# Performance work log

Measured on AMD Instinct MI355X. Metric: run time of the kernel, lower is better.

## Reference

```python
import jax, jax.numpy as jnp
import numpy as np

B, T, D_IN, D_H, N_H = 8, 1024, 512, 64, 8
PAD_TAIL = 128


def setup_inputs() -> dict:
    key = jax.random.key(0)
    ks = jax.random.split(key, 7)
    keys = jax.random.normal(ks[0], (B, T, D_IN), jnp.float32)
    queries = jax.random.normal(ks[1], (B, T, D_IN), jnp.float32)
    values = jax.random.normal(ks[2], (B, T, D_IN), jnp.float32)
    # truncated_normal(stddev=0.01) in the original; plain normal*0.01 is a faithful stand-in
    Wk = jax.random.normal(ks[3], (D_IN, D_H, N_H), jnp.float32) * 0.01
    Wq = jax.random.normal(ks[4], (D_IN, D_H, N_H), jnp.float32) * 0.01
    Wv = jax.random.normal(ks[5], (D_IN, D_H, N_H), jnp.float32) * 0.01
    key_seq = jax.random.randint(ks[6], (B, T), 0, 32000)
    key_seq = key_seq.at[:, -PAD_TAIL:].set(-1)  # -1 marks padding positions
    return {"keys": keys, "queries": queries, "values": values,
            "Wk": Wk, "Wq": Wq, "Wv": Wv, "key_seq": key_seq}


def reference(keys, queries, values, Wk, Wq, Wv, key_seq):
    # projections: (b, t, i) x (i, d, h) -> (b, t, d, h)
    Kh = jnp.einsum('bti,idh->btdh', keys, Wk)
    Qh = jnp.einsum('bti,idh->btdh', queries, Wq)
    Vh = jnp.einsum('bti,idh->btdh', values, Wv)

    # scores: i indexes keys, j indexes queries -> (b, Tk, Tq, h)
    scores = jnp.einsum('bidh,bjdh->bijh', Kh, Qh)

    dt = scores.dtype
    # padding mask over key positions (key_seq == -1 -> -1000)
    pad_mask = (-1000.0 * (1.0 - jnp.sign(key_seq + 1).astype(dt)))[:, :, None, None]
    # causal mask: disallow key index i > query index j (matrix_band_part(_, 0, -1) keeps i<=j)
    Tk, Tq = Kh.shape[1], Qh.shape[1]
    caus_mask = -1000.0 * jnp.tril(jnp.ones((Tk, Tq), dt), k=-1)
    mask = pad_mask + caus_mask[None, :, :, None]

    # NB: original adds mask BEFORE scaling, so the -1000 is also scaled. Keep that order.
    hidden_size = Kh.shape[2]
    scores = (scores + mask) / (hidden_size ** 0.5)

    # softmax over the key axis (axis=1)
    attn = jax.nn.softmax(scores, axis=1)

    # aggregate values: (b, i, j, h) x (b, i, d, h) -> (b, j, d, h)
    h_t = jnp.einsum('bijh,bidh->bjdh', attn, Vh)

    # tf.concat(tf.split(h_t, H, axis=-1), axis=2)[:, :, :, 0]
    # == per-head feature blocks laid out head-major along the feature axis
    b, j, d, nh = h_t.shape
    return h_t.transpose(0, 1, 3, 2).reshape(b, j, nh * d)
```

## Files before the change

### kernel.cpp

```cpp
#include <hip/hip_runtime.h>
#include <hip/hip_bf16.h>

#define B_SZ 8
#define T_SZ 1024
#define D_IN 512
#define D_H  64
#define N_H  8

typedef __hip_bfloat16 bf16;
using short8  = __attribute__((ext_vector_type(8))) short;
using short4v = __attribute__((ext_vector_type(4))) short;
using f32x4   = __attribute__((ext_vector_type(4))) float;

__device__ __forceinline__ unsigned short f2bf(float f) {
    union { __hip_bfloat16 b; unsigned short u; } c;
    c.b = __float2bfloat16(f);
    return c.u;
}

__global__ __launch_bounds__(256) void wt_kernel(
    const float* __restrict__ Wk, const float* __restrict__ Wq,
    const float* __restrict__ Wv, unsigned short* __restrict__ Wt)
{
    const int mat = blockIdx.y;
    const float* W = (mat == 0) ? Wk : (mat == 1) ? Wq : Wv;
    int idx = blockIdx.x * 256 + threadIdx.x;
    float v = W[idx];
    int k = idx >> 9, c = idx & 511;
    int h = c & 7, d = c >> 3;
    Wt[(((size_t)mat * 8 + h) * 64 + d) * 512 + k] = f2bf(v);
}

__global__ __launch_bounds__(256, 3) void proj_kernel(
    const float* __restrict__ keys, const float* __restrict__ queries,
    const float* __restrict__ values,
    const unsigned short* __restrict__ Wt, unsigned short* __restrict__ KQVb)
{
    const int tid = threadIdx.x;
    const int m0  = blockIdx.x * 128;
    const int n0  = blockIdx.y * 128;
    const int mat = blockIdx.z;

    const float* X = (mat == 0) ? keys : (mat == 1) ? queries : values;
    const unsigned short* WT = Wt + (size_t)mat * (512 * 512);
    unsigned short* P = KQVb + (size_t)mat * ((size_t)B_SZ * N_H * T_SZ * D_H);

    __shared__ __align__(16) unsigned short Xst[128 * 72];
    __shared__ __align__(16) unsigned short Wst[128 * 72];

    const int wid = tid >> 6, lane = tid & 63;
    const int quad = lane >> 4, l15 = lane & 15;
    const int wr = (wid >> 1) * 64, wc = (wid & 1) * 64;

    f32x4 acc[4][4];
    #pragma unroll
    for (int i = 0; i < 4; ++i)
        #pragma unroll
        for (int n = 0; n < 4; ++n) acc[i][n] = (f32x4){0.f, 0.f, 0.f, 0.f};

    const float4* X4 = (const float4*)X;

    for (int kc = 0; kc < 8; ++kc) {
        const int k0 = kc * 64;
        __syncthreads();
        #pragma unroll
        for (int q2 = 0; q2 < 8; ++q2) {
            int e = tid + q2 * 256;
            int r = e >> 4, c4 = e & 15;
            float4 v = X4[(size_t)(m0 + r) * (D_IN / 4) + (k0 >> 2) + c4];
            short4v s = {(short)f2bf(v.x), (short)f2bf(v.y),
                         (short)f2bf(v.z), (short)f2bf(v.w)};
            *(short4v*)&Xst[r * 72 + c4 * 4] = s;
        }
        #pragma unroll
        for (int q2 = 0; q2 < 4; ++q2) {
            int e = tid + q2 * 256;
            int row = e >> 3, ch = e & 7;
            *(short8*)&Wst[row * 72 + ch * 8] =
                *(const short8*)&WT[(size_t)(n0 + row) * 512 + k0 + ch * 8];
        }
        __syncthreads();
        #pragma unroll
        for (int ic = 0; ic < 2; ++ic) {
            short8 af[4], bf[4];
            #pragma unroll
            for (int mt = 0; mt < 4; ++mt)
                af[mt] = *(const short8*)&Xst[(wr + mt*16 + l15) * 72 + ic*32 + quad*8];
            #pragma unroll
            for (int nt = 0; nt < 4; ++nt)
                bf[nt] = *(const short8*)&Wst[(wc + nt*16 + l15) * 72 + ic*32 + quad*8];
            #pragma unroll
            for (int mt = 0; mt < 4; ++mt)
                #pragma unroll
                for (int nt = 0; nt < 4; ++nt)
                    acc[mt][nt] = __builtin_amdgcn_mfma_f32_16x16x32_bf16(
                        af[mt], bf[nt], acc[mt][nt], 0, 0, 0);
        }
    }

    #pragma unroll
    for (int mt = 0; mt < 4; ++mt)
        #pragma unroll
        for (int r = 0; r < 4; ++r) {
            int mrow = m0 + wr + mt * 16 + quad * 4 + r;
            int bb = mrow >> 10, t = mrow & 1023;
            #pragma unroll
            for (int nt = 0; nt < 4; ++nt) {
                int c = n0 + wc + nt * 16 + l15;
                int h = c >> 6, d = c & 63;
                P[(((size_t)(bb * N_H + h)) * T_SZ + t) * D_H + d] =
                    f2bf(acc[mt][nt][r]);
            }
        }
}

#define SCALE  0.18033688f
#define MASKV -180.33688f

__global__ __launch_bounds__(512, 4) void attn_kernel(
    const unsigned short* __restrict__ Qb, const unsigned short* __restrict__ Kb,
    const unsigned short* __restrict__ Vb,
    const int* __restrict__ key_seq, float* __restrict__ out)
{
    const int tid  = threadIdx.x;
    const int bid  = blockIdx.x;
    const int pair = bid >> 6;
    const int b    = (bid >> 3) & 7;
    const int h    = bid & 7;
    const int wid  = tid >> 6, lane = tid & 63;
    const int quad = lane >> 4, l15 = lane & 15;

    __shared__ __align__(16) unsigned short Kst[2][64 * 72];
    __shared__ __align__(16) unsigned short VTst[2][64 * 72];
    __shared__ __align__(16) float spadf[2][64];
    __shared__ int tflags[16];

    const size_t bh = (size_t)(b * N_H + h) * T_SZ;

    const int strip_j0 = (wid < 4) ? (15 - pair) * 64 : pair * 64;
    const int j0w = strip_j0 + (wid & 3) * 16;
    const int jg  = j0w + l15;
    const int ntmax = 16 - pair;

    short8 qf0 = *(const short8*)&Qb[(bh + jg) * D_H + quad * 8];
    short8 qf1 = *(const short8*)&Qb[(bh + jg) * D_H + 32 + quad * 8];

    {
        int ka  = key_seq[b * T_SZ + wid * 64 + lane];
        int kb2 = key_seq[b * T_SZ + 512 + wid * 64 + lane];
        unsigned long long ba  = __ballot(ka  != -1);
        unsigned long long bb2 = __ballot(kb2 != -1);
        if (lane == 0) {
            tflags[wid]     = (ba  != 0ull ? 1 : 0) | (ba  != ~0ull ? 2 : 0);
            tflags[8 + wid] = (bb2 != 0ull ? 1 : 0) | (bb2 != ~0ull ? 2 : 0);
        }
    }

    const int sk_row = tid >> 3, sk_c = tid & 7;
    const int sv_i = lane, sv_ch = wid;
    const int sv_col = (sv_i & 3) | ((sv_i & 16) >> 2) | ((sv_i & 4) << 1)
                     | ((sv_i & 8) << 1) | (sv_i & 32);

    short8 kreg = *(const short8*)&Kb[(bh + sk_row) * D_H + sk_c * 8];
    short8 vreg = *(const short8*)&Vb[(bh + sv_i) * D_H + sv_ch * 8];
    int ksv = (tid < 64) ? key_seq[b * T_SZ + tid] : -1;

    __syncthreads();

    unsigned tmask = 1u, pmask = 0u;
    #pragma unroll
    for (int t = 0; t < 16; ++t) {
        int f = tflags[t];
        tmask |= (unsigned)(f & 1) << t;
        pmask |= (unsigned)((f >> 1) & 1) << t;
    }
    tmask &= (unsigned)((1ull << ntmax) - 1ull);
    tmask |= 1u;

    *(short8*)&Kst[0][sk_row * 72 + sk_c * 8] = kreg;
    #pragma unroll
    for (int e = 0; e < 8; ++e)
        VTst[0][(sv_ch * 8 + e) * 72 + sv_col] = (unsigned short)vreg[e];
    if (tid < 64) spadf[0][tid] = (ksv == -1) ? MASKV : 0.f;
    __syncthreads();

    float m = -1e30f, l = 0.f;
    f32x4 o0 = {0.f,0.f,0.f,0.f}, o1 = o0, o2 = o0, o3 = o0;

    unsigned rem = tmask & ~1u;
    int tcur = 0, nb = 0;
    for (;;) {
        int tnext = -1;
        if (rem) { tnext = __ffs((int)rem) - 1; rem &= rem - 1; }
        if (tnext >= 0) {
            const size_t r0 = bh + tnext * 64;
            kreg = *(const short8*)&Kb[(r0 + sk_row) * D_H + sk_c * 8];
            vreg = *(const short8*)&Vb[(r0 + sv_i) * D_H + sv_ch * 8];
            if (tid < 64) ksv = key_seq[b * T_SZ + tnext * 64 + tid];
        }

        const int i0 = tcur * 64;
        if (i0 <= j0w + 15) {
            const bool haspad = (pmask >> tcur) & 1u;
            const bool needC  = (i0 + 63 > j0w);
            float sv[16];
            #pragma unroll
            for (int it = 0; it < 4; ++it) {
                f32x4 s = {0.f,0.f,0.f,0.f};
                short8 a0 = *(const short8*)&Kst[nb][(it*16 + l15) * 72 + quad*8];
                s = __builtin_amdgcn_mfma_f32_16x16x32_bf16(a0, qf0, s, 0, 0, 0);
                short8 a1 = *(const short8*)&Kst[nb][(it*16 + l15) * 72 + 32 + quad*8];
                s = __builtin_amdgcn_mfma_f32_16x16x32_bf16(a1, qf1, s, 0, 0, 0);
                f32x4 sp = {0.f,0.f,0.f,0.f};
                if (haspad) sp = *(const f32x4*)&spadf[nb][it*16 + quad*4];
                #pragma unroll
                for (int r = 0; r < 4; ++r) {
                    float v = __builtin_fmaf(s[r], SCALE, sp[r]);
                    if (needC && (i0 + it*16 + quad*4 + r > jg)) v += MASKV;
                    sv[it*4 + r] = v;
                }
            }

            float mt = sv[0];
            #pragma unroll
            for (int k = 1; k < 16; ++k) mt = fmaxf(mt, sv[k]);
            mt = fmaxf(mt, __shfl_xor(mt, 16));
            mt = fmaxf(mt, __shfl_xor(mt, 32));
            const float mnew  = fmaxf(m, mt);
            const float alpha = exp2f(m - mnew);
            float p[16], ls = 0.f;
            #pragma unroll
            for (int k = 0; k < 16; ++k) {
                p[k] = exp2f(sv[k] - mnew);
                ls += p[k];
            }
            ls += __shfl_xor(ls, 16);
            ls += __shfl_xor(ls, 32);
            l = l * alpha + ls;
            m = mnew;
            o0 *= alpha; o1 *= alpha; o2 *= alpha; o3 *= alpha;

            short8 pf0, pf1;
            #pragma unroll
            for (int e = 0; e < 8; ++e) {
                pf0[e] = (short)f2bf(p[e]);
                pf1[e] = (short)f2bf(p[8 + e]);
            }
            short8 a;
            a = *(const short8*)&VTst[nb][(     l15) * 72 +      quad * 8];
            o0 = __builtin_amdgcn_mfma_f32_16x16x32_bf16(a, pf0, o0, 0, 0, 0);
            a = *(const short8*)&VTst[nb][(     l15) * 72 + 32 + quad * 8];
            o0 = __builtin_amdgcn_mfma_f32_16x16x32_bf16(a, pf1, o0, 0, 0, 0);
            a = *(const short8*)&VTst[nb][(16 + l15) * 72 +      quad * 8];
            o1 = __builtin_amdgcn_mfma_f32_16x16x32_bf16(a, pf0, o1, 0, 0, 0);
            a = *(const short8*)&VTst[nb][(16 + l15) * 72 + 32 + quad * 8];
            o1 = __builtin_amdgcn_mfma_f32_16x16x32_bf16(a, pf1, o1, 0, 0, 0);
            a = *(const short8*)&VTst[nb][(32 + l15) * 72 +      quad * 8];
            o2 = __builtin_amdgcn_mfma_f32_16x16x32_bf16(a, pf0, o2, 0, 0, 0);
            a = *(const short8*)&VTst[nb][(32 + l15) * 72 + 32 + quad * 8];
            o2 = __builtin_amdgcn_mfma_f32_16x16x32_bf16(a, pf1, o2, 0, 0, 0);
            a = *(const short8*)&VTst[nb][(48 + l15) * 72 +      quad * 8];
            o3 = __builtin_amdgcn_mfma_f32_16x16x32_bf16(a, pf0, o3, 0, 0, 0);
            a = *(const short8*)&VTst[nb][(48 + l15) * 72 + 32 + quad * 8];
            o3 = __builtin_amdgcn_mfma_f32_16x16x32_bf16(a, pf1, o3, 0, 0, 0);
        }

        if (tnext < 0) break;

        const int nb2 = nb ^ 1;
        *(short8*)&Kst[nb2][sk_row * 72 + sk_c * 8] = kreg;
        #pragma unroll
        for (int e = 0; e < 8; ++e)
            VTst[nb2][(sv_ch * 8 + e) * 72 + sv_col] = (unsigned short)vreg[e];
        if (tid < 64) spadf[nb2][tid] = (ksv == -1) ? MASKV : 0.f;
        __syncthreads();
        tcur = tnext; nb = nb2;
    }

    const float inv = 1.f / l;
    float* op = out + ((size_t)b * T_SZ + jg) * (N_H * D_H) + h * D_H + quad * 4;
    *(f32x4*)(op +  0) = o0 * inv;
    *(f32x4*)(op + 16) = o1 * inv;
    *(f32x4*)(op + 32) = o2 * inv;
    *(f32x4*)(op + 48) = o3 * inv;
}

extern "C" void kernel_launch(void* const* d_in, const int* in_sizes, int n_in,
                              void* d_out, int out_size, void* d_ws, size_t ws_size,
                              hipStream_t stream) {
    const float* keys    = (const float*)d_in[0];
    const float* queries = (const float*)d_in[1];
    const float* values  = (const float*)d_in[2];
    const float* Wk      = (const float*)d_in[3];
    const float* Wq      = (const float*)d_in[4];
    const float* Wv      = (const float*)d_in[5];
    const int*   key_seq = (const int*)d_in[6];

    const size_t per = (size_t)B_SZ * N_H * T_SZ * D_H;
    unsigned short* KQVb = (unsigned short*)d_ws;
    unsigned short* Kb = KQVb;
    unsigned short* Qb = KQVb + per;
    unsigned short* Vb = KQVb + 2 * per;
    unsigned short* Wt = KQVb + 3 * per;

    wt_kernel<<<dim3(512 * 512 / 256, 3), 256, 0, stream>>>(Wk, Wq, Wv, Wt);
    proj_kernel<<<dim3(64, 4, 3), 256, 0, stream>>>(
        keys, queries, values, Wt, KQVb);
    attn_kernel<<<dim3(512), dim3(512), 0, stream>>>(
        Qb, Kb, Vb, key_seq, (float*)d_out);
}
```

Measured before the change: 156.5 us.

## Double-buffer projection GEMM with direct-to-LDS weight loads and swizzled LDS

Restructures the projection GEMM main loop. Weight tiles now go straight from global memory to a double-buffered LDS tile via global_load_lds, and the next X tile is prefetched into registers while the current tile is being computed. The padded LDS rows are replaced by an XOR swizzle, and the weight transpose kernel pre-swizzles its output so the direct copies land in the matching layout. This aims to hide global load latency and cut LDS footprint and bank conflicts, at the cost of more registers and reliance on vmcnt ordering, since only lgkmcnt is waited on explicitly before the barrier.

```diff
diff --git a/kernel.cpp b/kernel.cpp
--- a/kernel.cpp
+++ b/kernel.cpp
@@ -16,6 +16,12 @@
     union { __hip_bfloat16 b; unsigned short u; } c;
     c.b = __float2bfloat16(f);
     return c.u;
+}
+
+__device__ __forceinline__ void glds16(const unsigned short* g, unsigned short* l) {
+    __builtin_amdgcn_global_load_lds(
+        (const __attribute__((address_space(1))) unsigned int*)g,
+        (__attribute__((address_space(3))) unsigned int*)l, 16, 0, 0);
 }
 
 __global__ __launch_bounds__(256) void wt_kernel(
@@ -28,7 +34,8 @@
     float v = W[idx];
     int k = idx >> 9, c = idx & 511;
     int h = c & 7, d = c >> 3;
-    Wt[(((size_t)mat * 8 + h) * 64 + d) * 512 + k] = f2bf(v);
+    int ks = (k & ~63) | ((k & 63) ^ ((d & 7) << 3));
+    Wt[(((size_t)mat * 8 + h) * 64 + d) * 512 + ks] = f2bf(v);
 }
 
 __global__ __launch_bounds__(256, 3) void proj_kernel(
@@ -45,13 +52,17 @@
     const unsigned short* WT = Wt + (size_t)mat * (512 * 512);
     unsigned short* P = KQVb + (size_t)mat * ((size_t)B_SZ * N_H * T_SZ * D_H);
 
-    __shared__ __align__(16) unsigned short Xst[128 * 72];
-    __shared__ __align__(16) unsigned short Wst[128 * 72];
+    __shared__ __align__(16) unsigned short Xst[128 * 64];
+    __shared__ __align__(16) unsigned short Wst[2][128 * 64];
 
     const int wid = tid >> 6, lane = tid & 63;
     const int quad = lane >> 4, l15 = lane & 15;
     const int wr = (wid >> 1) * 64, wc = (wid & 1) * 64;
 
+    const int ur = tid >> 3, uch = tid & 7;
+    const int wrow  = wid * 32 + (lane >> 3);
+    const int wcol8 = (lane & 7) * 8;
+
     f32x4 acc[4][4];
     #pragma unroll
     for (int i = 0; i < 4; ++i)
@@ -60,42 +71,71 @@
 
     const float4* X4 = (const float4*)X;
 
+    #pragma unroll
+    for (int q = 0; q < 4; ++q)
+        glds16(&WT[(size_t)(n0 + wrow + q * 8) * 512 + wcol8],
+               &Wst[0][(wid * 4 + q) * 512]);
+    float4 xr[4][2];
+    #pragma unroll
+    for (int q = 0; q < 4; ++q) {
+        int r = ur + q * 32;
+        xr[q][0] = X4[(size_t)(m0 + r) * 128 + uch * 2];
+        xr[q][1] = X4[(size_t)(m0 + r) * 128 + uch * 2 + 1];
+    }
+
+    int wb = 0;
     for (int kc = 0; kc < 8; ++kc) {
-        const int k0 = kc * 64;
-        __syncthreads();
-        #pragma unroll
-        for (int q2 = 0; q2 < 8; ++q2) {
-            int e = tid + q2 * 256;
-            int r = e >> 4, c4 = e & 15;
-            float4 v = X4[(size_t)(m0 + r) * (D_IN / 4) + (k0 >> 2) + c4];
-            short4v s = {(short)f2bf(v.x), (short)f2bf(v.y),
-                         (short)f2bf(v.z), (short)f2bf(v.w)};
-            *(short4v*)&Xst[r * 72 + c4 * 4] = s;
-        }
-        #pragma unroll
-        for (int q2 = 0; q2 < 4; ++q2) {
-            int e = tid + q2 * 256;
-            int row = e >> 3, ch = e & 7;
-            *(short8*)&Wst[row * 72 + ch * 8] =
-                *(const short8*)&WT[(size_t)(n0 + row) * 512 + k0 + ch * 8];
-        }
-        __syncthreads();
+        #pragma unroll
+        for (int q = 0; q < 4; ++q) {
+            int r = ur + q * 32;
+            float4 a = xr[q][0], b = xr[q][1];
+            short8 s8 = {(short)f2bf(a.x), (short)f2bf(a.y),
+                         (short)f2bf(a.z), (short)f2bf(a.w),
+                         (short)f2bf(b.x), (short)f2bf(b.y),
+                         (short)f2bf(b.z), (short)f2bf(b.w)};
+            *(short8*)&Xst[r * 64 + ((uch * 8) ^ ((r & 7) << 3))] = s8;
+        }
+        if (kc < 7) {
+            const int k0n = (kc + 1) * 64;
+            #pragma unroll
+            for (int q = 0; q < 4; ++q)
+                glds16(&WT[(size_t)(n0 + wrow + q * 8) * 512 + k0n + wcol8],
+                       &Wst[wb ^ 1][(wid * 4 + q) * 512]);
+            #pragma unroll
+            for (int q = 0; q < 4; ++q) {
+                int r = ur + q * 32;
+                xr[q][0] = X4[(size_t)(m0 + r) * 128 + (k0n >> 2) + uch * 2];
+                xr[q][1] = X4[(size_t)(m0 + r) * 128 + (k0n >> 2) + uch * 2 + 1];
+            }
+        }
+        asm volatile("s_waitcnt lgkmcnt(0)" ::: "memory");
+        __builtin_amdgcn_s_barrier();
+
         #pragma unroll
         for (int ic = 0; ic < 2; ++ic) {
-            short8 af[4], bf[4];
-            #pragma unroll
-            for (int mt = 0; mt < 4; ++mt)
-                af[mt] = *(const short8*)&Xst[(wr + mt*16 + l15) * 72 + ic*32 + quad*8];
-            #pragma unroll
-            for (int nt = 0; nt < 4; ++nt)
-                bf[nt] = *(const short8*)&Wst[(wc + nt*16 + l15) * 72 + ic*32 + quad*8];
+            const int sc = ic * 32 + quad * 8;
+            short8 af[4], bfr[4];
+            #pragma unroll
+            for (int mt = 0; mt < 4; ++mt) {
+                int r = wr + mt * 16 + l15;
+                af[mt] = *(const short8*)&Xst[r * 64 + (sc ^ ((r & 7) << 3))];
+            }
+            #pragma unroll
+            for (int nt = 0; nt < 4; ++nt) {
+                int r = wc + nt * 16 + l15;
+                bfr[nt] = *(const short8*)&Wst[wb][r * 64 + (sc ^ ((r & 7) << 3))];
+            }
             #pragma unroll
             for (int mt = 0; mt < 4; ++mt)
                 #pragma unroll
                 for (int nt = 0; nt < 4; ++nt)
                     acc[mt][nt] = __builtin_amdgcn_mfma_f32_16x16x32_bf16(
-                        af[mt], bf[nt], acc[mt][nt], 0, 0, 0);
-        }
+                        af[mt], bfr[nt], acc[mt][nt], 0, 0, 0);
+        }
+
+        asm volatile("s_waitcnt lgkmcnt(0)" ::: "memory");
+        __builtin_amdgcn_s_barrier();
+        wb ^= 1;
     }
 
     #pragma unroll
```

Result: faster. 153.2 us (-2.1%).
